# Kernel optimization log

Hardware: AMD Instinct MI355X
Metric: run time of the kernel (lower is better)

The kernel has to match this reference:

```python
import jax, jax.numpy as jnp
import numpy as np

B = 64        # number of graphs
NPG = 2048    # nodes per graph (equal-size; math identical to padded ragged original)
N = B * NPG
C = 64        # in_channels == out_channels
H = 4         # num_heads
D = 64        # out_channels per head


def setup_inputs() -> dict:
    key = jax.random.key(0)
    k1, k2, k3, k4, k5 = jax.random.split(key, 5)
    s = 1.0 / np.sqrt(C)
    return {
        "x": jax.random.normal(k1, (N, C), dtype=jnp.float32),
        "Wq_w": jax.random.uniform(k2, (H * D, C), jnp.float32, -s, s),
        "Wq_b": jax.random.uniform(k3, (H * D,), jnp.float32, -s, s),
        "Wk_w": jax.random.uniform(k4, (H * D, C), jnp.float32, -s, s),
        "Wk_b": jax.random.uniform(k5, (H * D,), jnp.float32, -s, s),
        "n_nodes": jnp.full((B,), NPG, dtype=jnp.int32),
    }


def reference(x, Wq_w, Wq_b, Wk_w, Wk_b, n_nodes):
    # Linear projections (torch Linear: x @ W^T + b), reshape to [N, H, D]
    q = (x @ Wq_w.T + Wq_b).reshape(N, H, D)
    k = (x @ Wk_w.T + Wk_b).reshape(N, H, D)
    v = jnp.broadcast_to(x[:, None, :], (N, H, C))  # value = x repeated per head

    # L2-normalize q, k along feature dim
    q = q / jnp.linalg.norm(q, axis=2, keepdims=True)
    k = k / jnp.linalg.norm(k, axis=2, keepdims=True)

    # segment views: [B, n, H, D]
    qb = q.reshape(B, NPG, H, D)
    kb = k.reshape(B, NPG, H, D)
    vb = v.reshape(B, NPG, H, C)

    # per-graph k^T v outer product: [B, H, D, C]
    kv = jnp.einsum('bnhd,bnhe->bhde', kb, vb)
    k_sum = kb.sum(axis=1)  # [B, H, D]
    v_sum = vb.sum(axis=1)  # [B, H, C]

    numerator = jnp.einsum('bnhd,bhde->bnhe', qb, kv) + v_sum[:, None]  # [B, n, H, C]
    nn = n_nodes.astype(x.dtype)
    denominator = jnp.einsum('bnhd,bhd->bnh', qb, k_sum) + nn[:, None, None]  # [B, n, H]

    out = numerator / denominator[..., None]
    return out.reshape(N, H * C)
```

## Files before the change

kernel.cpp:

```cpp
#include <hip/hip_runtime.h>

#define NPG    2048
#define XP     72
#define TP     136
#define KVTSZ  6400

typedef short bf16x8 __attribute__((ext_vector_type(8)));
typedef float f32x4  __attribute__((ext_vector_type(4)));
typedef unsigned short u16x8 __attribute__((ext_vector_type(8)));
typedef unsigned short u16x4 __attribute__((ext_vector_type(4)));

__device__ __forceinline__ unsigned short f2b(float f) {
    unsigned int u = __float_as_uint(f);
    return (unsigned short)((u + 0x7FFFu + ((u >> 16) & 1u)) >> 16);
}

extern "C" __global__ __launch_bounds__(512, 4)
void kv_kernel(const float* __restrict__ x,
               const float* __restrict__ Wk_w,
               const float* __restrict__ Wk_b,
               float* __restrict__ kvt)
{
    __shared__ __align__(16) unsigned short wlds[64 * XP];
    __shared__ __align__(16) unsigned short xlds[128 * XP];
    __shared__ __align__(16) unsigned short xt[80 * TP];
    __shared__ __align__(16) unsigned short kt[80 * TP];

    const int t  = threadIdx.x;
    const int l  = t & 63;
    const int w  = t >> 6;
    const int lr = l & 15;
    const int lg = l >> 4;
    const int g    = blockIdx.x;
    const int xcd  = g & 7;
    const int rest = g >> 3;
    const int bhi  = rest & 7;
    const int h     = (rest >> 3) & 3;
    const int chunk = rest >> 5;
    const int b     = bhi * 8 + xcd;
    const int bh    = b * 4 + h;

    for (int idx = t; idx < 64 * 64; idx += 512) {
        int r = idx >> 6, c = idx & 63;
        wlds[r * XP + c] = f2b(Wk_w[(size_t)(h * 64 + r) * 64 + c]);
    }
    float bias[4][4];
#pragma unroll
    for (int mt = 0; mt < 4; ++mt)
#pragma unroll
        for (int i = 0; i < 4; ++i) bias[mt][i] = Wk_b[h * 64 + mt * 16 + 4 * lg + i];

    for (int idx = t; idx < 16 * TP; idx += 512) {
        int rr = idx / TP;
        int cc = idx - rr * TP;
        unsigned short v = (rr == 0 && cc < 128) ? (unsigned short)0x3F80u : (unsigned short)0u;
        xt[(64 + rr) * TP + cc] = v;
        kt[(64 + rr) * TP + cc] = v;
    }

    int cts[4], dts[4];
#pragma unroll
    for (int ti = 0; ti < 3; ++ti) {
        int tau = w + 8 * ti;
        int q5  = tau / 5;
        cts[ti] = q5;
        dts[ti] = tau - 5 * q5;
    }
    cts[3] = 4; dts[3] = 4;

    f32x4 kvacc[4] = {};
    const int cp = l | (w & 4) << 4;
    const int cpc = t & 63;
    const int n0  = (t >> 6) * 16;
    (void)cp;

    const float4* xg0 = (const float4*)(x + ((size_t)b * NPG + (size_t)chunk * 1024) * 64);

    float4 rx[4];
#pragma unroll
    for (int j = 0; j < 4; ++j) rx[j] = xg0[j * 512 + t];
#pragma unroll
    for (int j = 0; j < 4; ++j) {
        int n = j * 32 + (t >> 4), c = (t & 15) * 4;
        u16x4 pv = { f2b(rx[j].x), f2b(rx[j].y), f2b(rx[j].z), f2b(rx[j].w) };
        *(u16x4*)&xlds[n * XP + c] = pv;
    }
    __syncthreads();

    for (int tt = 0; tt < 8; ++tt) {
        {
            u16x8 w0, w1;
#pragma unroll
            for (int k2 = 0; k2 < 8; ++k2) w0[k2] = xlds[(n0 + k2) * XP + cpc];
#pragma unroll
            for (int k2 = 0; k2 < 8; ++k2) w1[k2] = xlds[(n0 + 8 + k2) * XP + cpc];
            *(u16x8*)&xt[cpc * TP + n0]     = w0;
            *(u16x8*)&xt[cpc * TP + n0 + 8] = w1;
        }

        f32x4 pacc[4] = {};
        const int ncol = w * 16 + lr;
#pragma unroll
        for (int ks = 0; ks < 2; ++ks) {
            bf16x8 xb = *(const bf16x8*)&xlds[ncol * XP + ks * 32 + lg * 8];
#pragma unroll
            for (int mt = 0; mt < 4; ++mt) {
                bf16x8 wfr = *(const bf16x8*)&wlds[(mt * 16 + lr) * XP + ks * 32 + lg * 8];
                pacc[mt] = __builtin_amdgcn_mfma_f32_16x16x32_bf16(wfr, xb, pacc[mt], 0, 0, 0);
            }
        }
        float ss = 0.f;
#pragma unroll
        for (int mt = 0; mt < 4; ++mt)
#pragma unroll
            for (int i = 0; i < 4; ++i) {
                float v = pacc[mt][i] + bias[mt][i];
                pacc[mt][i] = v;
                ss = fmaf(v, v, ss);
            }
        ss += __shfl_xor(ss, 16, 64);
        ss += __shfl_xor(ss, 32, 64);
        float sc = rsqrtf(ss);
#pragma unroll
        for (int mt = 0; mt < 4; ++mt)
#pragma unroll
            for (int i = 0; i < 4; ++i)
                kt[(mt * 16 + 4 * lg + i) * TP + ncol] = f2b(pacc[mt][i] * sc);
        __syncthreads();

        const bool more = (tt + 1) < 8;
        if (more) {
            const float4* xg = xg0 + (size_t)(tt + 1) * 128 * 16;
#pragma unroll
            for (int j = 0; j < 4; ++j) rx[j] = xg[j * 512 + t];
        }

#pragma unroll
        for (int ks = 0; ks < 4; ++ks) {
            const int ko = ks * 32 + lg * 8;
            bf16x8 a0 = *(const bf16x8*)&xt[(cts[0] * 16 + lr) * TP + ko];
            bf16x8 b0 = *(const bf16x8*)&kt[(dts[0] * 16 + lr) * TP + ko];
            kvacc[0] = __builtin_amdgcn_mfma_f32_16x16x32_bf16(a0, b0, kvacc[0], 0, 0, 0);
            bf16x8 a1 = *(const bf16x8*)&xt[(cts[1] * 16 + lr) * TP + ko];
            bf16x8 b1 = *(const bf16x8*)&kt[(dts[1] * 16 + lr) * TP + ko];
            kvacc[1] = __builtin_amdgcn_mfma_f32_16x16x32_bf16(a1, b1, kvacc[1], 0, 0, 0);
            bf16x8 a2 = *(const bf16x8*)&xt[(cts[2] * 16 + lr) * TP + ko];
            bf16x8 b2 = *(const bf16x8*)&kt[(dts[2] * 16 + lr) * TP + ko];
            kvacc[2] = __builtin_amdgcn_mfma_f32_16x16x32_bf16(a2, b2, kvacc[2], 0, 0, 0);
            if (w == 0) {
                bf16x8 a3 = *(const bf16x8*)&xt[(64 + lr) * TP + ko];
                bf16x8 b3 = *(const bf16x8*)&kt[(64 + lr) * TP + ko];
                kvacc[3] = __builtin_amdgcn_mfma_f32_16x16x32_bf16(a3, b3, kvacc[3], 0, 0, 0);
            }
        }

        if (more) {
#pragma unroll
            for (int j = 0; j < 4; ++j) {
                int n = j * 32 + (t >> 4), c = (t & 15) * 4;
                u16x4 pv = { f2b(rx[j].x), f2b(rx[j].y), f2b(rx[j].z), f2b(rx[j].w) };
                *(u16x4*)&xlds[n * XP + c] = pv;
            }
        }
        __syncthreads();
    }

    float* base = kvt + (size_t)(chunk * 256 + bh) * KVTSZ;
#pragma unroll
    for (int ti = 0; ti < 3; ++ti) {
        float* dst = base + (size_t)(cts[ti] * 16 + 4 * lg) * 80 + dts[ti] * 16 + lr;
#pragma unroll
        for (int i = 0; i < 4; ++i) dst[i * 80] = kvacc[ti][i];
    }
    if (w == 0) {
        float* dst = base + (size_t)(64 + 4 * lg) * 80 + 64 + lr;
#pragma unroll
        for (int i = 0; i < 4; ++i) dst[i * 80] = kvacc[3][i];
    }
}

extern "C" __global__ __launch_bounds__(256, 3)
void out_kernel(const float* __restrict__ x,
                const float* __restrict__ Wq_w,
                const float* __restrict__ Wq_b,
                const int* __restrict__ n_nodes,
                const float* __restrict__ kvt,
                float* __restrict__ out)
{
    __shared__ __align__(16) unsigned short wlds[64 * XP];
    __shared__ __align__(16) unsigned short xlds[64 * XP];
    __shared__ __align__(16) unsigned short qlds[64 * XP];

    const int t  = threadIdx.x;
    const int l  = t & 63;
    const int w  = t >> 6;
    const int lr = l & 15;
    const int lg = l >> 4;
    const int g    = blockIdx.x;
    const int xcd  = g & 7;
    const int rest = g >> 3;
    const int bhi  = rest & 7;
    const int h     = (rest >> 3) & 3;
    const int chunk = rest >> 5;
    const int b     = bhi * 8 + xcd;
    const int bh    = b * 4 + h;

    for (int idx = t; idx < 64 * 64; idx += 256) {
        int r = idx >> 6, c = idx & 63;
        wlds[r * XP + c] = f2b(Wq_w[(size_t)(h * 64 + r) * 64 + c]);
    }
    float bias[4][4];
#pragma unroll
    for (int mt = 0; mt < 4; ++mt)
#pragma unroll
        for (int i = 0; i < 4; ++i) bias[mt][i] = Wq_b[h * 64 + mt * 16 + 4 * lg + i];

    const float* kp0 = kvt + (size_t)bh * KVTSZ;
    const float* kp1 = kp0 + (size_t)256 * KVTSZ;
    bf16x8 kvf[4][2];
#pragma unroll
    for (int ct = 0; ct < 4; ++ct)
#pragma unroll
        for (int ks = 0; ks < 2; ++ks) {
            const int o = (ct * 16 + lr) * 80 + ks * 32 + lg * 8;
            bf16x8 f;
#pragma unroll
            for (int j = 0; j < 8; ++j) f[j] = (short)f2b(kp0[o + j] + kp1[o + j]);
            kvf[ct][ks] = f;
        }
    float ksr[4][4];
#pragma unroll
    for (int mt = 0; mt < 4; ++mt)
#pragma unroll
        for (int i = 0; i < 4; ++i) {
            const int d = mt * 16 + 4 * lg + i;
            ksr[mt][i] = kp0[64 * 80 + d] + kp1[64 * 80 + d];
        }
    float vsr[4];
#pragma unroll
    for (int ct = 0; ct < 4; ++ct) {
        const int o = (ct * 16 + lr) * 80 + 64;
        vsr[ct] = kp0[o] + kp1[o];
    }
    const float npg = (float)n_nodes[b];

    const float4* xg0 = (const float4*)(x + ((size_t)b * NPG + (size_t)chunk * 512) * 64);

    float4 rx[4];
#pragma unroll
    for (int j = 0; j < 4; ++j) rx[j] = xg0[j * 256 + t];
#pragma unroll
    for (int j = 0; j < 4; ++j) {
        int n = j * 16 + (t >> 4), c = (t & 15) * 4;
        u16x4 pv = { f2b(rx[j].x), f2b(rx[j].y), f2b(rx[j].z), f2b(rx[j].w) };
        *(u16x4*)&xlds[n * XP + c] = pv;
    }
    __syncthreads();

    for (int tt = 0; tt < 8; ++tt) {
        f32x4 pacc[4] = {};
        const int ncol = w * 16 + lr;
#pragma unroll
        for (int ks = 0; ks < 2; ++ks) {
            bf16x8 xb = *(const bf16x8*)&xlds[ncol * XP + ks * 32 + lg * 8];
#pragma unroll
            for (int mt = 0; mt < 4; ++mt) {
                bf16x8 wfr = *(const bf16x8*)&wlds[(mt * 16 + lr) * XP + ks * 32 + lg * 8];
                pacc[mt] = __builtin_amdgcn_mfma_f32_16x16x32_bf16(wfr, xb, pacc[mt], 0, 0, 0);
            }
        }
        float ss = 0.f, dd = 0.f;
#pragma unroll
        for (int mt = 0; mt < 4; ++mt)
#pragma unroll
            for (int i = 0; i < 4; ++i) {
                float v = pacc[mt][i] + bias[mt][i];
                pacc[mt][i] = v;
                ss = fmaf(v, v, ss);
                dd = fmaf(v, ksr[mt][i], dd);
            }
        ss += __shfl_xor(ss, 16, 64);
        ss += __shfl_xor(ss, 32, 64);
        dd += __shfl_xor(dd, 16, 64);
        dd += __shfl_xor(dd, 32, 64);
        float sc  = rsqrtf(ss);
        float den = fmaf(dd, sc, npg);
#pragma unroll
        for (int mt = 0; mt < 4; ++mt)
#pragma unroll
            for (int i = 0; i < 4; ++i)
                qlds[ncol * XP + mt * 16 + 4 * lg + i] = f2b(pacc[mt][i] * sc);
        __syncthreads();

        const bool more = (tt + 1) < 8;
        if (more) {
            const float4* xg = xg0 + (size_t)(tt + 1) * 64 * 16;
#pragma unroll
            for (int j = 0; j < 4; ++j) rx[j] = xg[j * 256 + t];
        }

        f32x4 nacc[4] = {};
#pragma unroll
        for (int ks = 0; ks < 2; ++ks) {
            bf16x8 qa = *(const bf16x8*)&qlds[(w * 16 + lr) * XP + ks * 32 + lg * 8];
#pragma unroll
            for (int ct = 0; ct < 4; ++ct)
                nacc[ct] = __builtin_amdgcn_mfma_f32_16x16x32_bf16(qa, kvf[ct][ks], nacc[ct], 0, 0, 0);
        }

        const size_t row0 = (size_t)b * NPG + (size_t)chunk * 512 + (size_t)tt * 64 + w * 16;
        float* op = out + row0 * 256 + h * 64;
#pragma unroll
        for (int i = 0; i < 4; ++i) {
            float den_i = __shfl(den, 4 * lg + i, 64);
            float rd = 1.0f / den_i;
#pragma unroll
            for (int ct = 0; ct < 4; ++ct)
                op[(size_t)(4 * lg + i) * 256 + ct * 16 + lr] = (nacc[ct][i] + vsr[ct]) * rd;
        }

        if (more) {
#pragma unroll
            for (int j = 0; j < 4; ++j) {
                int n = j * 16 + (t >> 4), c = (t & 15) * 4;
                u16x4 pv = { f2b(rx[j].x), f2b(rx[j].y), f2b(rx[j].z), f2b(rx[j].w) };
                *(u16x4*)&xlds[n * XP + c] = pv;
            }
        }
        __syncthreads();
    }
}

extern "C" void kernel_launch(void* const* d_in, const int* in_sizes, int n_in,
                              void* d_out, int out_size, void* d_ws, size_t ws_size,
                              hipStream_t stream) {
    const float* x     = (const float*)d_in[0];
    const float* Wq_w  = (const float*)d_in[1];
    const float* Wq_b  = (const float*)d_in[2];
    const float* Wk_w  = (const float*)d_in[3];
    const float* Wk_b  = (const float*)d_in[4];
    const int* n_nodes = (const int*)d_in[5];
    float* out = (float*)d_out;
    float* kvt = (float*)d_ws;

    hipLaunchKernelGGL(kv_kernel,  dim3(512),  dim3(512), 0, stream, x, Wk_w, Wk_b, kvt);
    hipLaunchKernelGGL(out_kernel, dim3(1024), dim3(256), 0, stream, x, Wq_w, Wq_b, n_nodes, kvt, out);
}
```

Measured before the change: 224.8 us.

## Make out_kernel waves independent: direct x fragment loads and shuffle-based q transpose

Each wave in out_kernel now owns its own 128-row chunk. It loads x directly from global memory into MFMA B-fragments instead of staging through LDS. The normalized q tile is moved into A-operand layout with cross-lane shuffles instead of a round-trip through a qlds buffer, which removes both per-iteration block barriers and two LDS arrays. The cost is more shuffle instructions, uncoalesced-ish 32-byte global loads per lane, no explicit prefetch of the next x tile, and the min-blocks launch bound is dropped.

```diff
diff --git a/kernel.cpp b/kernel.cpp
--- a/kernel.cpp
+++ b/kernel.cpp
@@ -69,10 +69,8 @@
     cts[3] = 4; dts[3] = 4;
 
     f32x4 kvacc[4] = {};
-    const int cp = l | (w & 4) << 4;
     const int cpc = t & 63;
     const int n0  = (t >> 6) * 16;
-    (void)cp;
 
     const float4* xg0 = (const float4*)(x + ((size_t)b * NPG + (size_t)chunk * 1024) * 64);
 
@@ -179,7 +177,7 @@
     }
 }
 
-extern "C" __global__ __launch_bounds__(256, 3)
+extern "C" __global__ __launch_bounds__(256)
 void out_kernel(const float* __restrict__ x,
                 const float* __restrict__ Wq_w,
                 const float* __restrict__ Wq_b,
@@ -188,8 +186,6 @@
                 float* __restrict__ out)
 {
     __shared__ __align__(16) unsigned short wlds[64 * XP];
-    __shared__ __align__(16) unsigned short xlds[64 * XP];
-    __shared__ __align__(16) unsigned short qlds[64 * XP];
 
     const int t  = threadIdx.x;
     const int l  = t & 63;
@@ -198,16 +194,18 @@
     const int lg = l >> 4;
     const int g    = blockIdx.x;
     const int xcd  = g & 7;
-    const int rest = g >> 3;
-    const int bhi  = rest & 7;
-    const int h     = (rest >> 3) & 3;
-    const int chunk = rest >> 5;
-    const int b     = bhi * 8 + xcd;
-    const int bh    = b * 4 + h;
+    const int r    = g >> 3;
+    const int bhi  = r & 7;
+    const int hq   = r >> 3;
+    const int h    = hq & 3;
+    const int quarter = hq >> 2;
+    const int b    = bhi * 8 + xcd;
+    const int bh   = b * 4 + h;
+    const int chunk = quarter * 4 + w;
 
     for (int idx = t; idx < 64 * 64; idx += 256) {
-        int r = idx >> 6, c = idx & 63;
-        wlds[r * XP + c] = f2b(Wq_w[(size_t)(h * 64 + r) * 64 + c]);
+        int rr = idx >> 6, c = idx & 63;
+        wlds[rr * XP + c] = f2b(Wq_w[(size_t)(h * 64 + rr) * 64 + c]);
     }
     float bias[4][4];
 #pragma unroll
@@ -244,31 +242,36 @@
     }
     const float npg = (float)n_nodes[b];
 
-    const float4* xg0 = (const float4*)(x + ((size_t)b * NPG + (size_t)chunk * 512) * 64);
-
-    float4 rx[4];
-#pragma unroll
-    for (int j = 0; j < 4; ++j) rx[j] = xg0[j * 256 + t];
-#pragma unroll
-    for (int j = 0; j < 4; ++j) {
-        int n = j * 16 + (t >> 4), c = (t & 15) * 4;
-        u16x4 pv = { f2b(rx[j].x), f2b(rx[j].y), f2b(rx[j].z), f2b(rx[j].w) };
-        *(u16x4*)&xlds[n * XP + c] = pv;
-    }
     __syncthreads();
 
-    for (int tt = 0; tt < 8; ++tt) {
+    const float* xbase = x + ((size_t)b * NPG + (size_t)chunk * 128) * 64;
+    const int src0 = lr + 16 * ((lg & 1) * 2);
+    const int src1 = src0 + 16;
+
+    for (int gg = 0; gg < 8; ++gg) {
+        const float* xr = xbase + (size_t)(gg * 16 + lr) * 64;
+        bf16x8 xb[2];
+#pragma unroll
+        for (int ks = 0; ks < 2; ++ks) {
+            float4 p0 = *(const float4*)(xr + ks * 32 + lg * 8);
+            float4 p1 = *(const float4*)(xr + ks * 32 + lg * 8 + 4);
+            bf16x8 f;
+            f[0] = (short)f2b(p0.x); f[1] = (short)f2b(p0.y);
+            f[2] = (short)f2b(p0.z); f[3] = (short)f2b(p0.w);
+            f[4] = (short)f2b(p1.x); f[5] = (short)f2b(p1.y);
+            f[6] = (short)f2b(p1.z); f[7] = (short)f2b(p1.w);
+            xb[ks] = f;
+        }
+
         f32x4 pacc[4] = {};
-        const int ncol = w * 16 + lr;
-#pragma unroll
-        for (int ks = 0; ks < 2; ++ks) {
-            bf16x8 xb = *(const bf16x8*)&xlds[ncol * XP + ks * 32 + lg * 8];
+#pragma unroll
+        for (int ks = 0; ks < 2; ++ks)
 #pragma unroll
             for (int mt = 0; mt < 4; ++mt) {
                 bf16x8 wfr = *(const bf16x8*)&wlds[(mt * 16 + lr) * XP + ks * 32 + lg * 8];
-                pacc[mt] = __builtin_amdgcn_mfma_f32_16x16x32_bf16(wfr, xb, pacc[mt], 0, 0, 0);
-            }
-        }
+                pacc[mt] = __builtin_amdgcn_mfma_f32_16x16x32_bf16(wfr, xb[ks], pacc[mt], 0, 0, 0);
+            }
+
         float ss = 0.f, dd = 0.f;
 #pragma unroll
         for (int mt = 0; mt < 4; ++mt)
@@ -283,51 +286,51 @@
         ss += __shfl_xor(ss, 32, 64);
         dd += __shfl_xor(dd, 16, 64);
         dd += __shfl_xor(dd, 32, 64);
-        float sc  = rsqrtf(ss);
-        float den = fmaf(dd, sc, npg);
+        const float sc  = rsqrtf(ss);
+        const float den = fmaf(dd, sc, npg);
+
+        unsigned pw[4][2];
+#pragma unroll
+        for (int mt = 0; mt < 4; ++mt) {
+            pw[mt][0] = (unsigned)f2b(pacc[mt][0] * sc) | ((unsigned)f2b(pacc[mt][1] * sc) << 16);
+            pw[mt][1] = (unsigned)f2b(pacc[mt][2] * sc) | ((unsigned)f2b(pacc[mt][3] * sc) << 16);
+        }
+
+        unsigned r0[4][2], r1[4][2];
 #pragma unroll
         for (int mt = 0; mt < 4; ++mt)
 #pragma unroll
-            for (int i = 0; i < 4; ++i)
-                qlds[ncol * XP + mt * 16 + 4 * lg + i] = f2b(pacc[mt][i] * sc);
-        __syncthreads();
-
-        const bool more = (tt + 1) < 8;
-        if (more) {
-            const float4* xg = xg0 + (size_t)(tt + 1) * 64 * 16;
-#pragma unroll
-            for (int j = 0; j < 4; ++j) rx[j] = xg[j * 256 + t];
-        }
+            for (int p = 0; p < 2; ++p) {
+                r0[mt][p] = __shfl(pw[mt][p], src0, 64);
+                r1[mt][p] = __shfl(pw[mt][p], src1, 64);
+            }
+        const bool hi = (lg >> 1) & 1;
+        union { unsigned u[4]; bf16x8 v; } a0, a1;
+        a0.u[0] = hi ? r0[1][0] : r0[0][0];
+        a0.u[1] = hi ? r0[1][1] : r0[0][1];
+        a0.u[2] = hi ? r1[1][0] : r1[0][0];
+        a0.u[3] = hi ? r1[1][1] : r1[0][1];
+        a1.u[0] = hi ? r0[3][0] : r0[2][0];
+        a1.u[1] = hi ? r0[3][1] : r0[2][1];
+        a1.u[2] = hi ? r1[3][0] : r1[2][0];
+        a1.u[3] = hi ? r1[3][1] : r1[2][1];
 
         f32x4 nacc[4] = {};
 #pragma unroll
-        for (int ks = 0; ks < 2; ++ks) {
-            bf16x8 qa = *(const bf16x8*)&qlds[(w * 16 + lr) * XP + ks * 32 + lg * 8];
-#pragma unroll
-            for (int ct = 0; ct < 4; ++ct)
-                nacc[ct] = __builtin_amdgcn_mfma_f32_16x16x32_bf16(qa, kvf[ct][ks], nacc[ct], 0, 0, 0);
-        }
-
-        const size_t row0 = (size_t)b * NPG + (size_t)chunk * 512 + (size_t)tt * 64 + w * 16;
-        float* op = out + row0 * 256 + h * 64;
+        for (int ct = 0; ct < 4; ++ct) {
+            nacc[ct] = __builtin_amdgcn_mfma_f32_16x16x32_bf16(a0.v, kvf[ct][0], nacc[ct], 0, 0, 0);
+            nacc[ct] = __builtin_amdgcn_mfma_f32_16x16x32_bf16(a1.v, kvf[ct][1], nacc[ct], 0, 0, 0);
+        }
+
+        float* op = out + ((size_t)b * NPG + (size_t)chunk * 128 + gg * 16) * 256 + h * 64;
 #pragma unroll
         for (int i = 0; i < 4; ++i) {
-            float den_i = __shfl(den, 4 * lg + i, 64);
-            float rd = 1.0f / den_i;
+            const float den_i = __shfl(den, 4 * lg + i, 64);
+            const float rd = 1.0f / den_i;
 #pragma unroll
             for (int ct = 0; ct < 4; ++ct)
                 op[(size_t)(4 * lg + i) * 256 + ct * 16 + lr] = (nacc[ct][i] + vsr[ct]) * rd;
         }
-
-        if (more) {
-#pragma unroll
-            for (int j = 0; j < 4; ++j) {
-                int n = j * 16 + (t >> 4), c = (t & 15) * 4;
-                u16x4 pv = { f2b(rx[j].x), f2b(rx[j].y), f2b(rx[j].z), f2b(rx[j].w) };
-                *(u16x4*)&xlds[n * XP + c] = pv;
-            }
-        }
-        __syncthreads();
     }
 }
 
```

After: 223.7 us. No clear change (-0.5%).
